# Performance work log

Hardware: AMD Instinct MI355X
Metric: run time of the kernel (lower is better)

The kernel has to match this reference:

```python
import jax, jax.numpy as jnp
import numpy as np

B, H, S, D = 1, 16, 4096, 64


def setup_inputs() -> dict:
    key = jax.random.key(0)
    kq, kk, kv = jax.random.split(key, 3)
    Q = jax.random.normal(kq, (B, H, S, D), dtype=jnp.float32)
    K = jax.random.normal(kk, (B, H, S, D), dtype=jnp.float32)
    V = jax.random.normal(kv, (B, H, S, D), dtype=jnp.float32)
    # causal mask, broadcast over batch/heads: True = attend
    mask = jnp.tril(jnp.ones((S, S), dtype=bool))[None, None, :, :]
    return {"Q": Q, "K": K, "V": V, "mask": mask}


def reference(Q, K, V, mask):
    d_k = Q.shape[-1]
    scale = 1.0 / jnp.sqrt(jnp.asarray(d_k, dtype=Q.dtype))
    # [..., q, k] scores; mask==False positions set to -inf before softmax
    scores = jnp.einsum('...qd,...kd->...qk', Q, K) * scale
    scores = jnp.where(mask, scores, jnp.asarray(-jnp.inf, dtype=scores.dtype))
    attn = jax.nn.softmax(scores, axis=-1)
    return jnp.einsum('...qk,...kd->...qd', attn, V)
```

## Files before the change

kernel.cpp:

```cpp
#include <hip/hip_runtime.h>
#include <hip/hip_bf16.h>

typedef __attribute__((ext_vector_type(8))) short short8;
typedef __attribute__((ext_vector_type(4))) short s4v;
typedef __attribute__((ext_vector_type(2))) int   int2v;
typedef __attribute__((ext_vector_type(4))) float floatx4;

#define MFMA16(A,B,C) __builtin_amdgcn_mfma_f32_16x16x32_bf16(A,B,C,0,0,0)
#define LDS_FENCE() asm volatile("s_waitcnt lgkmcnt(0)" ::: "memory")

__device__ __forceinline__ short bf16bits(float x) {
    __hip_bfloat16 h = __float2bfloat16(x);
    return *(short*)&h;
}
__device__ __forceinline__ short8 cvt8(const float* p) {
    floatx4 a = *(const floatx4*)p;
    floatx4 b = *(const floatx4*)(p + 4);
    short8 r;
    r[0]=bf16bits(a.x); r[1]=bf16bits(a.y); r[2]=bf16bits(a.z); r[3]=bf16bits(a.w);
    r[4]=bf16bits(b.x); r[5]=bf16bits(b.y); r[6]=bf16bits(b.z); r[7]=bf16bits(b.w);
    return r;
}
__device__ __forceinline__ short8 cvt8s(const float* p) {
    constexpr float SCL2 = 0.125f * 1.44269504088896f;
    floatx4 a = *(const floatx4*)p;
    floatx4 b = *(const floatx4*)(p + 4);
    a *= SCL2; b *= SCL2;
    short8 r;
    r[0]=bf16bits(a.x); r[1]=bf16bits(a.y); r[2]=bf16bits(a.z); r[3]=bf16bits(a.w);
    r[4]=bf16bits(b.x); r[5]=bf16bits(b.y); r[6]=bf16bits(b.z); r[7]=bf16bits(b.w);
    return r;
}
__device__ __forceinline__ int pk2(float lo, float hi) {
    int r;
    asm("v_cvt_pk_bf16_f32 %0, %1, %2" : "=v"(r) : "v"(lo), "v"(hi));
    return r;
}

__global__ __launch_bounds__(256) void prep(const float* __restrict__ V,
                                            short* __restrict__ VT,
                                            const float* __restrict__ K,
                                            short* __restrict__ K16, int doK)
{
    __shared__ short tile[64 * 65];
    const int t  = threadIdx.x;
    const int h  = blockIdx.x >> 6;
    const int s0 = (blockIdx.x & 63) << 6;
    const float* src = V + ((size_t)h * 4096 + s0) * 64;
    const int r = t >> 4, dq = (t & 15) * 4;
#pragma unroll
    for (int pass = 0; pass < 4; ++pass) {
        const int s = pass * 16 + r;
        floatx4 f = *(const floatx4*)(src + s * 64 + dq);
        short* w = tile + s * 65 + dq;
        w[0] = bf16bits(f.x); w[1] = bf16bits(f.y);
        w[2] = bf16bits(f.z); w[3] = bf16bits(f.w);
    }
    __syncthreads();
    const int d = t >> 2, sc = (t & 3) * 16;
    short8 a, b;
#pragma unroll
    for (int j = 0; j < 8; ++j) a[j] = tile[(sc + j) * 65 + d];
#pragma unroll
    for (int j = 0; j < 8; ++j) b[j] = tile[(sc + 8 + j) * 65 + d];
    short* dst = VT + ((size_t)h * 64 + d) * 4096 + s0 + sc;
    *(short8*)dst       = a;
    *(short8*)(dst + 8) = b;
    if (doK) {
        const size_t base = (size_t)blockIdx.x * 4096 + (size_t)t * 16;
        *(short8*)(K16 + base)     = cvt8(K + base);
        *(short8*)(K16 + base + 8) = cvt8(K + base + 8);
    }
}

template<bool KB16>
__global__ __launch_bounds__(256, 2)
void attn_fast(const float* __restrict__ Qg, const float* __restrict__ Kg,
               const short* __restrict__ K16g, const short* __restrict__ VTg,
               float* __restrict__ Og)
{
    constexpr int S = 4096, D = 64;

    __shared__ __align__(16) short lK[4096];
    __shared__ __align__(16) short lV[4096];
    __shared__ __align__(16) short lP[8192];

    const int tid = threadIdx.x;
    const int wv  = tid >> 6;
    const int ln  = tid & 63;
    const int ll  = ln & 15;
    const int qd  = ln >> 4;

    const int c = blockIdx.x & 255;
    const int s = blockIdx.x >> 8;
    const int h = c & 15;
    const int x = c >> 4;
    const int qblk = (s == 0) ? (31 - x) : x;
    const int qb   = qblk << 7;
    const int qrow = qb + wv * 32;

    const float* Qh  = Qg  + (size_t)h * S * D;
    const float* Kf  = Kg  + (size_t)h * S * D;
    const short* K16 = K16g + (size_t)h * S * D;
    const short* Vt  = VTg + (size_t)h * 64 * S;

    short8 qA0, qA1, qB0, qB1;
    {
        const float* qp = Qh + (qrow + ll) * D + qd * 8;
        qA0 = cvt8s(qp);       qA1 = cvt8s(qp + 32);
        const float* qp2 = qp + 16 * D;
        qB0 = cvt8s(qp2);      qB1 = cvt8s(qp2 + 32);
    }

    floatx4 oA[4], oB[4], olA, olB;
#pragma unroll
    for (int dt = 0; dt < 4; ++dt) { oA[dt] = (floatx4){0.f,0.f,0.f,0.f}; oB[dt] = oA[dt]; }
    olA = (floatx4){0.f,0.f,0.f,0.f};
    olB = olA;

    short8 ones;
#pragma unroll
    for (int j = 0; j < 8; ++j) ones[j] = (short)0x3F80;

    const int kkey = tid >> 3, kd8 = tid & 7;
    const int koct = kd8 & 3;
    short* kdst = lK + ((kkey >> 4) * 2 + (kd8 >> 2)) * 512
                     + ((((kkey & 15) | (koct << 4)) ^ (koct * 5)) * 8);
    const float* ksrcf = Kf  + kkey * 64 + kd8 * 8;
    const short* ksrc6 = K16 + kkey * 64 + kd8 * 8;
    const int vd = tid >> 2, voct = tid & 3;
    short* vdst = lV + (vd >> 4) * 512
                     + ((((vd & 15) | (voct << 4)) ^ (voct * 5)) * 8);
    const short* vsrc = Vt + (size_t)vd * S + voct * 8;
    const int rblk = ((ll | (qd << 4)) ^ (qd * 5));
    const int pswz  = (ll >> 1) & 3;
    short* lPw = lP + wv * 2048;
    const int pw0 = ll * 32 + (((qd >> 1) ^ pswz) * 8) + (qd & 1) * 4;
    const int prd = ll * 32 + ((qd ^ pswz) * 8);

    const int kv_end = qb + 128;
    const int wv_end = qrow + 32;

    auto ldK = [&](int kv) -> short8 {
        return KB16 ? *(const short8*)(ksrc6 + kv * 64) : cvt8(ksrcf + kv * 64);
    };

    short8 kpre0 = ldK(0),  kpre1 = ldK(32);
    short8 vpre0 = *(const short8*)(vsrc);
    short8 vpre1 = *(const short8*)(vsrc + 32);

#define SOFTMAX_STORE(S0, S1, QG, BASE, KVH) do {                              \
    float p0_[4], p1_[4];                                                      \
    _Pragma("unroll")                                                          \
    for (int r = 0; r < 4; ++r) { p0_[r] = exp2f((S0)[r]); p1_[r] = exp2f((S1)[r]); } \
    if ((KVH) + 31 > (QG)) {                                                   \
        const int qg_ = (QG) + ll;                                             \
        const int k0_ = (KVH) + qd * 4, k1_ = k0_ + 16;                        \
        _Pragma("unroll")                                                      \
        for (int r = 0; r < 4; ++r) {                                          \
            if (k0_ + r > qg_) p0_[r] = 0.f;                                   \
            if (k1_ + r > qg_) p1_[r] = 0.f;                                   \
        }                                                                      \
    }                                                                          \
    *(int2v*)((BASE) + pw0)        = (int2v){pk2(p0_[0],p0_[1]), pk2(p0_[2],p0_[3])}; \
    *(int2v*)((BASE) + (pw0 ^ 16)) = (int2v){pk2(p1_[0],p1_[1]), pk2(p1_[2],p1_[3])}; \
} while (0)

    for (int kv = 0; kv < kv_end; kv += 64) {
        __syncthreads();
        *(short8*)kdst          = kpre0;
        *(short8*)(kdst + 2048) = kpre1;
        *(short8*)vdst          = vpre0;
        *(short8*)(vdst + 2048) = vpre1;
        __syncthreads();
        if (kv + 64 < kv_end) {
            kpre0 = ldK(kv + 64);
            kpre1 = ldK(kv + 96);
            vpre0 = *(const short8*)(vsrc + kv + 64);
            vpre1 = *(const short8*)(vsrc + kv + 96);
        }

        if (kv < wv_end) {
            const bool h1 = (kv + 32 < wv_end);
            floatx4 zz = (floatx4){0.f,0.f,0.f,0.f};
            floatx4 sA0=zz, sA1=zz, sA2=zz, sA3=zz;
            floatx4 sB0=zz, sB1=zz, sB2=zz, sB3=zz;
            short8 kf;
            __builtin_amdgcn_s_setprio(1);
            kf = ((const short8*)(lK +    0))[rblk]; sA0 = MFMA16(kf, qA0, sA0); sB0 = MFMA16(kf, qB0, sB0);
            kf = ((const short8*)(lK +  512))[rblk]; sA0 = MFMA16(kf, qA1, sA0); sB0 = MFMA16(kf, qB1, sB0);
            kf = ((const short8*)(lK + 1024))[rblk]; sA1 = MFMA16(kf, qA0, sA1); sB1 = MFMA16(kf, qB0, sB1);
            kf = ((const short8*)(lK + 1536))[rblk]; sA1 = MFMA16(kf, qA1, sA1); sB1 = MFMA16(kf, qB1, sB1);
            if (h1) {
                kf = ((const short8*)(lK + 2048))[rblk]; sA2 = MFMA16(kf, qA0, sA2); sB2 = MFMA16(kf, qB0, sB2);
                kf = ((const short8*)(lK + 2560))[rblk]; sA2 = MFMA16(kf, qA1, sA2); sB2 = MFMA16(kf, qB1, sB2);
                kf = ((const short8*)(lK + 3072))[rblk]; sA3 = MFMA16(kf, qA0, sA3); sB3 = MFMA16(kf, qB0, sB3);
                kf = ((const short8*)(lK + 3584))[rblk]; sA3 = MFMA16(kf, qA1, sA3); sB3 = MFMA16(kf, qB1, sB3);
            }
            __builtin_amdgcn_s_setprio(0);

            SOFTMAX_STORE(sA0, sA1, qrow,      lPw,        kv);
            SOFTMAX_STORE(sB0, sB1, qrow + 16, lPw + 1024, kv);
            if (h1) {
                SOFTMAX_STORE(sA2, sA3, qrow,      lPw + 512,  kv + 32);
                SOFTMAX_STORE(sB2, sB3, qrow + 16, lPw + 1536, kv + 32);
            }
            LDS_FENCE();

            short8 pfA = *(const short8*)(lPw + prd);
            short8 pfB = *(const short8*)(lPw + 1024 + prd);
            __builtin_amdgcn_s_setprio(1);
#pragma unroll
            for (int dt = 0; dt < 4; ++dt) {
                short8 vf = ((const short8*)(lV + dt * 512))[rblk];
                oA[dt] = MFMA16(pfA, vf, oA[dt]);
                oB[dt] = MFMA16(pfB, vf, oB[dt]);
            }
            olA = MFMA16(pfA, ones, olA);
            olB = MFMA16(pfB, ones, olB);
            __builtin_amdgcn_s_setprio(0);
            if (h1) {
                short8 pfA1 = *(const short8*)(lPw + 512 + prd);
                short8 pfB1 = *(const short8*)(lPw + 1536 + prd);
                __builtin_amdgcn_s_setprio(1);
#pragma unroll
                for (int dt = 0; dt < 4; ++dt) {
                    short8 vf = ((const short8*)(lV + 2048 + dt * 512))[rblk];
                    oA[dt] = MFMA16(pfA1, vf, oA[dt]);
                    oB[dt] = MFMA16(pfB1, vf, oB[dt]);
                }
                olA = MFMA16(pfA1, ones, olA);
                olB = MFMA16(pfB1, ones, olB);
                __builtin_amdgcn_s_setprio(0);
            }
        }
    }
#undef SOFTMAX_STORE

#pragma unroll
    for (int r = 0; r < 4; ++r) {
        const float rl = 1.f / fmaxf(olA[r], 1e-37f);
        const int q = qrow + qd * 4 + r;
        float* op = Og + ((size_t)h * S + q) * D + ll;
#pragma unroll
        for (int dt = 0; dt < 4; ++dt)
            op[dt * 16] = oA[dt][r] * rl;
    }
#pragma unroll
    for (int r = 0; r < 4; ++r) {
        const float rl = 1.f / fmaxf(olB[r], 1e-37f);
        const int q = qrow + 16 + qd * 4 + r;
        float* op = Og + ((size_t)h * S + q) * D + ll;
#pragma unroll
        for (int dt = 0; dt < 4; ++dt)
            op[dt * 16] = oB[dt][r] * rl;
    }
}

__global__ __launch_bounds__(256, 4)
void attn_legacy(const float* __restrict__ Qg, const float* __restrict__ Kg,
                 const float* __restrict__ Vg, float* __restrict__ Og)
{
    constexpr int S = 4096, D = 64;
    constexpr float SCL2 = 0.125f * 1.44269504088896f;
    constexpr float NEG  = -1.0e30f;
    __shared__ __align__(16) short lK[2048];
    __shared__ __align__(16) short lV[2048];
    __shared__ __align__(16) short lP[2048];
    const int tid = threadIdx.x, wv = tid >> 6, ln = tid & 63, ll = ln & 15, qd = ln >> 4;
    const int bid = blockIdx.x, h = bid & 15, qblk = 63 - (bid >> 4), qb = qblk << 6;
    const float* Qh = Qg + (size_t)h * S * D;
    const float* Kh = Kg + (size_t)h * S * D;
    const float* Vh = Vg + (size_t)h * S * D;
    const int qrow = qb + wv * 16;
    short8 qf0, qf1;
    { const float* qp = Qh + (qrow + ll) * D + qd * 8; qf0 = cvt8(qp); qf1 = cvt8(qp + 32); }
    floatx4 o[4]; float mi[4], li[4];
#pragma unroll
    for (int dt = 0; dt < 4; ++dt) o[dt] = (floatx4){0.f,0.f,0.f,0.f};
#pragma unroll
    for (int r = 0; r < 4; ++r) { mi[r] = NEG; li[r] = 0.f; }
    const int k_st = tid >> 3, dbase = (tid & 7) * 8;
    const int sq = (dbase >> 3) & 3, sks = dbase >> 5;
    const int kw_slot = (((k_st >> 4) * 2 + sks) * 64)
                      + (((sq << 4) | (k_st & 15)) ^ (sq | (sks << 2)));
    const int kr0 = ln ^ qd, kr1 = ln ^ (qd | 4), vbit3 = (ln >> 3) & 1;
    const int kv_end = qb + 64, wv_end = qrow + 16;
    for (int kv = 0; kv < kv_end; kv += 32) {
        __syncthreads();
        {
            short8 kval = cvt8(Kh + (kv + k_st) * D + dbase);
            ((short8*)lK)[kw_slot] = kval;
            short8 vval = cvt8(Vh + (kv + k_st) * D + dbase);
            const int vq = (k_st >> 3) << 4, vj = k_st & 7;
#pragma unroll
            for (int i = 0; i < 8; ++i) {
                int d = dbase + i, dt = d >> 4, l2 = d & 15;
                int lp = (vq | l2) ^ (((l2 >> 3) & 1) | (dt << 1));
                lV[dt * 512 + lp * 8 + vj] = vval[i];
            }
        }
        __syncthreads();
        if (kv < wv_end) {
            floatx4 sc0 = (floatx4){0.f,0.f,0.f,0.f}, sc1 = sc0; short8 kf;
            kf = ((const short8*)lK)[0*64+kr0]; sc0 = MFMA16(qf0, kf, sc0);
            kf = ((const short8*)lK)[1*64+kr1]; sc0 = MFMA16(qf1, kf, sc0);
            kf = ((const short8*)lK)[2*64+kr0]; sc1 = MFMA16(qf0, kf, sc1);
            kf = ((const short8*)lK)[3*64+kr1]; sc1 = MFMA16(qf1, kf, sc1);
            float p0[4], p1[4]; const int qg = qrow + qd * 4;
#pragma unroll
            for (int r = 0; r < 4; ++r) { p0[r] = sc0[r]*SCL2; p1[r] = sc1[r]*SCL2; }
            if (kv + 31 > qrow) {
                const int k0 = kv + ll, k1 = kv + 16 + ll;
#pragma unroll
                for (int r = 0; r < 4; ++r) {
                    if (k0 > qg + r) p0[r] = NEG;
                    if (k1 > qg + r) p1[r] = NEG;
                }
            }
#pragma unroll
            for (int r = 0; r < 4; ++r) {
                float mx = fmaxf(p0[r], p1[r]);
                mx = fmaxf(mx, __shfl_xor(mx,1)); mx = fmaxf(mx, __shfl_xor(mx,2));
                mx = fmaxf(mx, __shfl_xor(mx,4)); mx = fmaxf(mx, __shfl_xor(mx,8));
                const float nm = fmaxf(mi[r], mx);
                const float a = exp2f(mi[r] - nm); mi[r] = nm;
                p0[r] = exp2f(p0[r] - nm); p1[r] = exp2f(p1[r] - nm);
                float ps = p0[r] + p1[r];
                ps += __shfl_xor(ps,1); ps += __shfl_xor(ps,2);
                ps += __shfl_xor(ps,4); ps += __shfl_xor(ps,8);
                li[r] = li[r] * a + ps;
#pragma unroll
                for (int dt = 0; dt < 4; ++dt) o[dt][r] *= a;
            }
            {
                const int pbase = wv * 512 + (ll & 7);
                const int dl0 = ((ll >> 3) << 4) + qd * 4;
#pragma unroll
                for (int r = 0; r < 4; ++r) {
                    lP[pbase + (dl0 + r) * 8]      = bf16bits(p0[r]);
                    lP[pbase + (dl0 + 32 + r) * 8] = bf16bits(p1[r]);
                }
            }
            __threadfence_block();
            short8 pf = ((const short8*)lP)[wv * 64 + ln];
#pragma unroll
            for (int dt = 0; dt < 4; ++dt) {
                short8 vf = ((const short8*)lV)[dt * 64 + (ln ^ (vbit3 | (dt << 1)))];
                o[dt] = MFMA16(pf, vf, o[dt]);
            }
        }
    }
#pragma unroll
    for (int r = 0; r < 4; ++r) {
        const float rl = 1.f / fmaxf(li[r], 1e-30f);
        const int q = qrow + qd * 4 + r;
        float* op = Og + ((size_t)h * S + q) * D + ll;
#pragma unroll
        for (int dt = 0; dt < 4; ++dt) op[dt * 16] = o[dt][r] * rl;
    }
}

extern "C" void kernel_launch(void* const* d_in, const int* in_sizes, int n_in,
                              void* d_out, int out_size, void* d_ws, size_t ws_size,
                              hipStream_t stream) {
    const float* Q = (const float*)d_in[0];
    const float* K = (const float*)d_in[1];
    const float* V = (const float*)d_in[2];
    float* O = (float*)d_out;
    const size_t elems  = (size_t)16 * 4096 * 64;
    const size_t oneBuf = elems * sizeof(short);
    if (ws_size >= 2 * oneBuf) {
        short* VT  = (short*)d_ws;
        short* K16 = (short*)d_ws + elems;
        prep<<<dim3(1024), dim3(256), 0, stream>>>(V, VT, K, K16, 1);
        attn_fast<true><<<dim3(512), dim3(256), 0, stream>>>(Q, K, K16, VT, O);
    } else if (ws_size >= oneBuf) {
        short* VT = (short*)d_ws;
        prep<<<dim3(1024), dim3(256), 0, stream>>>(V, VT, K, VT, 0);
        attn_fast<false><<<dim3(512), dim3(256), 0, stream>>>(Q, K, nullptr, VT, O);
    } else {
        attn_legacy<<<dim3(1024), dim3(256), 0, stream>>>(Q, K, V, O);
    }
}
```

Baseline: 223.8 us.

## Double-buffer K/V tiles via direct global-to-LDS loads and pair causal tiles

K and V tiles now go straight from global memory into a double-buffered LDS area with global_load_lds, instead of being staged through registers. This drops one of the two barriers per iteration and lets the next tile's loads overlap the current tile's compute. The work split also changes: each block takes one short and one long 64-row causal query tile (x and 63-x), with two waves on each, so every block gets the same amount of work. In exchange LDS use doubles, and waves on the short tile sit idle at barriers while the long tile finishes.

```diff
diff --git a/kernel.cpp b/kernel.cpp
--- a/kernel.cpp
+++ b/kernel.cpp
@@ -35,6 +35,11 @@
     int r;
     asm("v_cvt_pk_bf16_f32 %0, %1, %2" : "=v"(r) : "v"(lo), "v"(hi));
     return r;
+}
+__device__ __forceinline__ void g2l16(const short* g, short* l) {
+    __builtin_amdgcn_global_load_lds(
+        (const __attribute__((address_space(1))) void*)g,
+        (__attribute__((address_space(3))) void*)l, 16, 0, 0);
 }
 
 __global__ __launch_bounds__(256) void prep(const float* __restrict__ V,
@@ -81,8 +86,8 @@
 {
     constexpr int S = 4096, D = 64;
 
-    __shared__ __align__(16) short lK[4096];
-    __shared__ __align__(16) short lV[4096];
+    __shared__ __align__(16) short lK[8192];
+    __shared__ __align__(16) short lV[8192];
     __shared__ __align__(16) short lP[8192];
 
     const int tid = threadIdx.x;
@@ -92,12 +97,14 @@
     const int qd  = ln >> 4;
 
     const int c = blockIdx.x & 255;
+    const int h = c & 15;
+    const int t = c >> 4;
     const int s = blockIdx.x >> 8;
-    const int h = c & 15;
-    const int x = c >> 4;
-    const int qblk = (s == 0) ? (31 - x) : x;
-    const int qb   = qblk << 7;
-    const int qrow = qb + wv * 32;
+    const int x = s ? (31 - t) : t;
+    const int myTile = (wv < 2) ? (63 - x) : x;
+    const int qrow   = myTile * 64 + (wv & 1) * 32;
+    const int kv_end = (64 - x) * 64;
+    const int wv_end = qrow + 32;
 
     const float* Qh  = Qg  + (size_t)h * S * D;
     const float* Kf  = Kg  + (size_t)h * S * D;
@@ -122,32 +129,46 @@
 #pragma unroll
     for (int j = 0; j < 8; ++j) ones[j] = (short)0x3F80;
 
-    const int kkey = tid >> 3, kd8 = tid & 7;
-    const int koct = kd8 & 3;
-    short* kdst = lK + ((kkey >> 4) * 2 + (kd8 >> 2)) * 512
-                     + ((((kkey & 15) | (koct << 4)) ^ (koct * 5)) * 8);
-    const float* ksrcf = Kf  + kkey * 64 + kd8 * 8;
-    const short* ksrc6 = K16 + kkey * 64 + kd8 * 8;
-    const int vd = tid >> 2, voct = tid & 3;
-    short* vdst = lV + (vd >> 4) * 512
-                     + ((((vd & 15) | (voct << 4)) ^ (voct * 5)) * 8);
-    const short* vsrc = Vt + (size_t)vd * S + voct * 8;
+    int kOff0, kOff1, vOff0, vOff1, kKey0, kKey1, kD80, kD81;
+    {
+#pragma unroll
+        for (int j = 0; j < 2; ++j) {
+            const int slot = (wv * 2 + j) * 64 + ln;
+            const int hh = slot >> 8;
+            const int bb = (slot >> 6) & 3;
+            const int sw = slot & 63;
+            const int ko = (sw >> 4) & 3;
+            const int kkey = hh * 32 + (bb >> 1) * 16 + ((sw ^ (ko * 5)) & 15);
+            const int kd8  = ((bb & 1) << 2) | ko;
+            const int vo = ko;
+            const int vd = bb * 16 + ((sw ^ (vo * 5)) & 15);
+            const int kOf = kkey * 64 + kd8 * 8;
+            const int vOf = vd * S + hh * 32 + vo * 8;
+            if (j == 0) { kOff0 = kOf; vOff0 = vOf; kKey0 = kkey; kD80 = kd8; }
+            else        { kOff1 = kOf; vOff1 = vOf; kKey1 = kkey; kD81 = kd8; }
+        }
+    }
+    const int dstA = (wv * 2 + 0) * 512;
+    const int dstB = (wv * 2 + 1) * 512;
+
     const int rblk = ((ll | (qd << 4)) ^ (qd * 5));
     const int pswz  = (ll >> 1) & 3;
     short* lPw = lP + wv * 2048;
     const int pw0 = ll * 32 + (((qd >> 1) ^ pswz) * 8) + (qd & 1) * 4;
     const int prd = ll * 32 + ((qd ^ pswz) * 8);
 
-    const int kv_end = qb + 128;
-    const int wv_end = qrow + 32;
-
-    auto ldK = [&](int kv) -> short8 {
-        return KB16 ? *(const short8*)(ksrc6 + kv * 64) : cvt8(ksrcf + kv * 64);
-    };
-
-    short8 kpre0 = ldK(0),  kpre1 = ldK(32);
-    short8 vpre0 = *(const short8*)(vsrc);
-    short8 vpre1 = *(const short8*)(vsrc + 32);
+    short8 kApre, kBpre;
+    g2l16(Vt + vOff0, lV + dstA);
+    g2l16(Vt + vOff1, lV + dstB);
+    if (KB16) {
+        g2l16(K16 + kOff0, lK + dstA);
+        g2l16(K16 + kOff1, lK + dstB);
+    } else {
+        *(short8*)(lK + dstA) = cvt8(Kf + (size_t)kKey0 * D + kD80 * 8);
+        *(short8*)(lK + dstB) = cvt8(Kf + (size_t)kKey1 * D + kD81 * 8);
+        kApre = cvt8(Kf + (size_t)(64 + kKey0) * D + kD80 * 8);
+        kBpre = cvt8(Kf + (size_t)(64 + kKey1) * D + kD81 * 8);
+    }
 
 #define SOFTMAX_STORE(S0, S1, QG, BASE, KVH) do {                              \
     float p0_[4], p1_[4];                                                      \
@@ -166,36 +187,44 @@
     *(int2v*)((BASE) + (pw0 ^ 16)) = (int2v){pk2(p1_[0],p1_[1]), pk2(p1_[2],p1_[3])}; \
 } while (0)
 
+    int bo = 0;
     for (int kv = 0; kv < kv_end; kv += 64) {
         __syncthreads();
-        *(short8*)kdst          = kpre0;
-        *(short8*)(kdst + 2048) = kpre1;
-        *(short8*)vdst          = vpre0;
-        *(short8*)(vdst + 2048) = vpre1;
-        __syncthreads();
+        const int nbo = bo ^ 4096;
         if (kv + 64 < kv_end) {
-            kpre0 = ldK(kv + 64);
-            kpre1 = ldK(kv + 96);
-            vpre0 = *(const short8*)(vsrc + kv + 64);
-            vpre1 = *(const short8*)(vsrc + kv + 96);
+            g2l16(Vt + (kv + 64) + vOff0, lV + nbo + dstA);
+            g2l16(Vt + (kv + 64) + vOff1, lV + nbo + dstB);
+            if (KB16) {
+                g2l16(K16 + (size_t)(kv + 64) * 64 + kOff0, lK + nbo + dstA);
+                g2l16(K16 + (size_t)(kv + 64) * 64 + kOff1, lK + nbo + dstB);
+            } else {
+                *(short8*)(lK + nbo + dstA) = kApre;
+                *(short8*)(lK + nbo + dstB) = kBpre;
+                if (kv + 128 < kv_end) {
+                    kApre = cvt8(Kf + (size_t)(kv + 128 + kKey0) * D + kD80 * 8);
+                    kBpre = cvt8(Kf + (size_t)(kv + 128 + kKey1) * D + kD81 * 8);
+                }
+            }
         }
 
         if (kv < wv_end) {
             const bool h1 = (kv + 32 < wv_end);
+            const short* Kb = lK + bo;
+            const short* Vb = lV + bo;
             floatx4 zz = (floatx4){0.f,0.f,0.f,0.f};
             floatx4 sA0=zz, sA1=zz, sA2=zz, sA3=zz;
             floatx4 sB0=zz, sB1=zz, sB2=zz, sB3=zz;
             short8 kf;
             __builtin_amdgcn_s_setprio(1);
-            kf = ((const short8*)(lK +    0))[rblk]; sA0 = MFMA16(kf, qA0, sA0); sB0 = MFMA16(kf, qB0, sB0);
-            kf = ((const short8*)(lK +  512))[rblk]; sA0 = MFMA16(kf, qA1, sA0); sB0 = MFMA16(kf, qB1, sB0);
-            kf = ((const short8*)(lK + 1024))[rblk]; sA1 = MFMA16(kf, qA0, sA1); sB1 = MFMA16(kf, qB0, sB1);
-            kf = ((const short8*)(lK + 1536))[rblk]; sA1 = MFMA16(kf, qA1, sA1); sB1 = MFMA16(kf, qB1, sB1);
+            kf = ((const short8*)(Kb +    0))[rblk]; sA0 = MFMA16(kf, qA0, sA0); sB0 = MFMA16(kf, qB0, sB0);
+            kf = ((const short8*)(Kb +  512))[rblk]; sA0 = MFMA16(kf, qA1, sA0); sB0 = MFMA16(kf, qB1, sB0);
+            kf = ((const short8*)(Kb + 1024))[rblk]; sA1 = MFMA16(kf, qA0, sA1); sB1 = MFMA16(kf, qB0, sB1);
+            kf = ((const short8*)(Kb + 1536))[rblk]; sA1 = MFMA16(kf, qA1, sA1); sB1 = MFMA16(kf, qB1, sB1);
             if (h1) {
-                kf = ((const short8*)(lK + 2048))[rblk]; sA2 = MFMA16(kf, qA0, sA2); sB2 = MFMA16(kf, qB0, sB2);
-                kf = ((const short8*)(lK + 2560))[rblk]; sA2 = MFMA16(kf, qA1, sA2); sB2 = MFMA16(kf, qB1, sB2);
-                kf = ((const short8*)(lK + 3072))[rblk]; sA3 = MFMA16(kf, qA0, sA3); sB3 = MFMA16(kf, qB0, sB3);
-                kf = ((const short8*)(lK + 3584))[rblk]; sA3 = MFMA16(kf, qA1, sA3); sB3 = MFMA16(kf, qB1, sB3);
+                kf = ((const short8*)(Kb + 2048))[rblk]; sA2 = MFMA16(kf, qA0, sA2); sB2 = MFMA16(kf, qB0, sB2);
+                kf = ((const short8*)(Kb + 2560))[rblk]; sA2 = MFMA16(kf, qA1, sA2); sB2 = MFMA16(kf, qB1, sB2);
+                kf = ((const short8*)(Kb + 3072))[rblk]; sA3 = MFMA16(kf, qA0, sA3); sB3 = MFMA16(kf, qB0, sB3);
+                kf = ((const short8*)(Kb + 3584))[rblk]; sA3 = MFMA16(kf, qA1, sA3); sB3 = MFMA16(kf, qB1, sB3);
             }
             __builtin_amdgcn_s_setprio(0);
 
@@ -212,7 +241,7 @@
             __builtin_amdgcn_s_setprio(1);
 #pragma unroll
             for (int dt = 0; dt < 4; ++dt) {
-                short8 vf = ((const short8*)(lV + dt * 512))[rblk];
+                short8 vf = ((const short8*)(Vb + dt * 512))[rblk];
                 oA[dt] = MFMA16(pfA, vf, oA[dt]);
                 oB[dt] = MFMA16(pfB, vf, oB[dt]);
             }
@@ -225,7 +254,7 @@
                 __builtin_amdgcn_s_setprio(1);
 #pragma unroll
                 for (int dt = 0; dt < 4; ++dt) {
-                    short8 vf = ((const short8*)(lV + 2048 + dt * 512))[rblk];
+                    short8 vf = ((const short8*)(Vb + 2048 + dt * 512))[rblk];
                     oA[dt] = MFMA16(pfA1, vf, oA[dt]);
                     oB[dt] = MFMA16(pfB1, vf, oB[dt]);
                 }
@@ -234,6 +263,7 @@
                 __builtin_amdgcn_s_setprio(0);
             }
         }
+        bo = nbo;
     }
 #undef SOFTMAX_STORE
 
```

Result: slower. 252.5 us (+12.8%).
